# Kernel tuning notes

Hardware: AMD Instinct MI355X
Metric: run time of the kernel (lower is better)

The kernel has to match this reference:

```python
import jax, jax.numpy as jnp
import numpy as np

L, B, D = 50, 1024, 512      # memory slots, batch, d_model
H, DK = 4, 512               # heads, per-head dim (d_k = d_model in this module)
HOP = 3


def setup_inputs() -> dict:
    key = jax.random.key(0)
    ks = jax.random.split(key, 16)
    s = lambda i, shape: jax.random.normal(ks[i], shape, jnp.float32) * 0.02
    return dict(
        momery=jax.random.normal(ks[0], (L, B, D), jnp.float32),
        hid=jax.random.normal(ks[1], (B, D), jnp.float32),
        text_polarity=jax.random.normal(ks[2], (B,), jnp.float32),
        attribute_polarity=jax.random.normal(ks[3], (B,), jnp.float32),
        w=jnp.array(0.5, jnp.float32),
        p_w1=s(4, (D, D)), p_b1=jnp.zeros((D,), jnp.float32),
        p_w2=s(5, (D, D)), p_b2=jnp.zeros((D,), jnp.float32),
        wq=s(6, (D, H * DK)), bq=jnp.zeros((H * DK,), jnp.float32),
        wk=s(7, (D, H * DK)), bk=jnp.zeros((H * DK,), jnp.float32),
        wv=s(8, (D, H * DK)), bv=jnp.zeros((H * DK,), jnp.float32),
        wo=s(9, (H * DK, D)), bo=jnp.zeros((D,), jnp.float32),
    )


def reference(momery, hid, text_polarity, attribute_polarity, w,
              p_w1, p_b1, p_w2, p_b2, wq, bq, wk, bk, wv, bv, wo, bo):
    # k, v depend only on hid (attinkv = hid every hop/slot) -> hoist out of hop loop
    k = (hid @ wk + bk).reshape(B, H, DK)   # [B,H,DK]
    v = (hid @ wv + bv).reshape(B, H, DK)   # [B,H,DK]
    inv_sqrt_dk = jnp.float32(1.0 / np.sqrt(DK))
    for _ in range(HOP):
        # projection MLP over all slots at once (replaces per-slot loop)
        mid = jax.nn.relu(momery @ p_w1 + p_b1) @ p_w2 + p_b2          # [L,B,D]
        q = (mid @ wq + bq).reshape(L, B, H, DK)                        # [L,B,H,DK]
        # single key per query (nk=1): scores [L,B,H,1], softmax -> ones
        scores = (jnp.einsum('lbhd,bhd->lbh', q, k) * inv_sqrt_dk)[..., None]
        att = jax.nn.softmax(scores, axis=-1)                           # [L,B,H,1]
        out = att * v                                                   # [L,B,H,DK]
        temp = out.reshape(L, B, H * DK) @ wo + bo                      # [L,B,D]
        momery = momery + w * temp
    return momery
```

## Files before the change

### kernel.cpp

```cpp
#include <hip/hip_runtime.h>
#include <hip/hip_bf16.h>

typedef short short8 __attribute__((ext_vector_type(8)));
typedef float f4 __attribute__((ext_vector_type(4)));

__device__ __forceinline__ short f2bfs(float f) {
    __hip_bfloat16 h = __float2bfloat16(f);
    return __builtin_bit_cast(short, h);
}

__device__ __forceinline__ unsigned packbf2(float a, float b, float s) {
    unsigned lo = (unsigned short)f2bfs(s * a);
    unsigned hi = (unsigned short)f2bfs(s * b);
    return (hi << 16) | lo;
}

#define MFMA(a, b, c) __builtin_amdgcn_mfma_f32_16x16x32_bf16(a, b, c, 0, 0, 0)

__global__ __launch_bounds__(256) void gemmW(const float* __restrict__ wv,
                                             const float* __restrict__ wo,
                                             const float* __restrict__ bv,
                                             const float* __restrict__ bo,
                                             const float* __restrict__ w,
                                             short* __restrict__ WsT,
                                             float* __restrict__ b2p) {
    constexpr int K = 2048, N = 512, NT = 16;
    const int tid = threadIdx.x;
    const int bx  = blockIdx.x;

    if (bx >= 256) {
        const int g = (bx - 256) * 256 + tid;
        const int o = g & 511;
        const int r = g >> 9;
        float s = (r == 0) ? bo[o] : 0.f;
        const int j0 = r * 64;
#pragma unroll 8
        for (int j = j0; j < j0 + 64; ++j) s += bv[j] * wo[(size_t)j * N + o];
        b2p[r * 512 + o] = s;
        return;
    }

    __shared__ float red[4][32][33];

    const int row0 = (bx >> 4) * 32;
    const int col0 = (bx & 15) * 32;
    const int lane = tid & 63, wave = tid >> 6;
    const int ln = lane & 15, q = lane >> 4;
    const int k0 = wave * 512;

    const float* pa0 = wv + (size_t)(row0 + ln) * K + k0 + q * 8;
    const float* pa1 = pa0 + (size_t)16 * K;
    const float* pb  = wo + (size_t)(k0 + q * 8) * N;

    float4 a00 = *(const float4*)pa0, a01 = *(const float4*)(pa0 + 4);
    float4 a10 = *(const float4*)pa1, a11 = *(const float4*)(pa1 + 4);
    float b0r[8], b1r[8];
#pragma unroll
    for (int j = 0; j < 8; ++j) {
        b0r[j] = pb[(size_t)j * N + col0 + ln];
        b1r[j] = pb[(size_t)j * N + col0 + 16 + ln];
    }

    f4 acc00 = {0,0,0,0}, acc01 = {0,0,0,0}, acc10 = {0,0,0,0}, acc11 = {0,0,0,0};

    for (int t = 0; t < NT; ++t) {
        short8 af0, af1, bf0, bf1;
        af0[0]=f2bfs(a00.x); af0[1]=f2bfs(a00.y); af0[2]=f2bfs(a00.z); af0[3]=f2bfs(a00.w);
        af0[4]=f2bfs(a01.x); af0[5]=f2bfs(a01.y); af0[6]=f2bfs(a01.z); af0[7]=f2bfs(a01.w);
        af1[0]=f2bfs(a10.x); af1[1]=f2bfs(a10.y); af1[2]=f2bfs(a10.z); af1[3]=f2bfs(a10.w);
        af1[4]=f2bfs(a11.x); af1[5]=f2bfs(a11.y); af1[6]=f2bfs(a11.z); af1[7]=f2bfs(a11.w);
#pragma unroll
        for (int j = 0; j < 8; ++j) { bf0[j] = f2bfs(b0r[j]); bf1[j] = f2bfs(b1r[j]); }

        if (t + 1 < NT) {
            pa0 += 32; pa1 += 32; pb += (size_t)32 * N;
            a00 = *(const float4*)pa0; a01 = *(const float4*)(pa0 + 4);
            a10 = *(const float4*)pa1; a11 = *(const float4*)(pa1 + 4);
#pragma unroll
            for (int j = 0; j < 8; ++j) {
                b0r[j] = pb[(size_t)j * N + col0 + ln];
                b1r[j] = pb[(size_t)j * N + col0 + 16 + ln];
            }
        }
        acc00 = MFMA(af0, bf0, acc00); acc01 = MFMA(af0, bf1, acc01);
        acc10 = MFMA(af1, bf0, acc10); acc11 = MFMA(af1, bf1, acc11);
    }

#pragma unroll
    for (int r = 0; r < 4; ++r) {
        red[wave][q * 4 + r][ln]           = acc00[r];
        red[wave][q * 4 + r][ln + 16]      = acc01[r];
        red[wave][16 + q * 4 + r][ln]      = acc10[r];
        red[wave][16 + q * 4 + r][ln + 16] = acc11[r];
    }
    __syncthreads();

    const float wsc = 3.0f * w[0];
    const int n  = tid >> 3;
    const int d0 = (tid & 7) * 4;
    float s0 = red[0][d0][n]     + red[1][d0][n]     + red[2][d0][n]     + red[3][d0][n];
    float s1 = red[0][d0 + 1][n] + red[1][d0 + 1][n] + red[2][d0 + 1][n] + red[3][d0 + 1][n];
    float s2 = red[0][d0 + 2][n] + red[1][d0 + 2][n] + red[2][d0 + 2][n] + red[3][d0 + 2][n];
    float s3 = red[0][d0 + 3][n] + red[1][d0 + 3][n] + red[2][d0 + 3][n] + red[3][d0 + 3][n];
    short* p = WsT + (size_t)(col0 + n) * 512 + row0 + d0;
    *(unsigned*)p       = packbf2(s0, s1, wsc);
    *(unsigned*)(p + 2) = packbf2(s2, s3, wsc);
}

__global__ __launch_bounds__(256) void gemmT(const float* __restrict__ hid,
                                             const short* __restrict__ WsT,
                                             const float* __restrict__ b2p,
                                             const float* __restrict__ w,
                                             float* __restrict__ t) {
    constexpr int K = 512, N = 512, NT = 16;
    __shared__ float bred[4][64];

    const int tid  = threadIdx.x;
    const int col0 = blockIdx.x * 64;
    const int row0 = blockIdx.y * 32;
    const int lane = tid & 63, wave = tid >> 6;
    const int ln = lane & 15, q = lane >> 4;
    const int col = col0 + wave * 16 + ln;

    const int cl = tid & 63, rr = tid >> 6;
    const float* bpp = b2p + (size_t)(rr * 8) * 512 + col0 + cl;
    float bp = 0.f;
#pragma unroll
    for (int k = 0; k < 8; ++k) bp += bpp[(size_t)k * 512];

    const float* pa0 = hid + (size_t)(row0 + ln) * K + q * 8;
    const float* pa1 = pa0 + (size_t)16 * K;
    const short* pb  = WsT + (size_t)col * K + q * 8;

    float4 a00 = *(const float4*)pa0, a01 = *(const float4*)(pa0 + 4);
    float4 a10 = *(const float4*)pa1, a11 = *(const float4*)(pa1 + 4);
    short8 bf = *(const short8*)pb;

    f4 acc0 = {0,0,0,0}, acc1 = {0,0,0,0};

    for (int tt = 0; tt < NT; ++tt) {
        short8 af0, af1;
        af0[0]=f2bfs(a00.x); af0[1]=f2bfs(a00.y); af0[2]=f2bfs(a00.z); af0[3]=f2bfs(a00.w);
        af0[4]=f2bfs(a01.x); af0[5]=f2bfs(a01.y); af0[6]=f2bfs(a01.z); af0[7]=f2bfs(a01.w);
        af1[0]=f2bfs(a10.x); af1[1]=f2bfs(a10.y); af1[2]=f2bfs(a10.z); af1[3]=f2bfs(a10.w);
        af1[4]=f2bfs(a11.x); af1[5]=f2bfs(a11.y); af1[6]=f2bfs(a11.z); af1[7]=f2bfs(a11.w);
        short8 b = bf;
        if (tt + 1 < NT) {
            pa0 += 32; pa1 += 32; pb += 32;
            a00 = *(const float4*)pa0; a01 = *(const float4*)(pa0 + 4);
            a10 = *(const float4*)pa1; a11 = *(const float4*)(pa1 + 4);
            bf = *(const short8*)pb;
        }
        acc0 = MFMA(af0, b, acc0);
        acc1 = MFMA(af1, b, acc1);
    }

    bred[rr][cl] = bp;
    __syncthreads();
    const int lc = wave * 16 + ln;
    const float wsc  = 3.0f * w[0];
    const float bias = wsc * (bred[0][lc] + bred[1][lc] + bred[2][lc] + bred[3][lc]);

#pragma unroll
    for (int r = 0; r < 4; ++r) {
        t[(size_t)(row0 + q * 4 + r) * N + col]      = acc0[r] + bias;
        t[(size_t)(row0 + 16 + q * 4 + r) * N + col] = acc1[r] + bias;
    }
}

__global__ __launch_bounds__(256) void bcast(const float* __restrict__ mem,
                                             const float* __restrict__ t,
                                             float* __restrict__ out) {
    const size_t idx = (size_t)blockIdx.x * 256 + threadIdx.x;
    const int bd4 = (int)(idx & (131072 - 1));
    const f4 tv = ((const f4*)t)[bd4];
    const f4 m  = ((const f4*)mem)[idx];
    ((f4*)out)[idx] = m + tv;
}

extern "C" void kernel_launch(void* const* d_in, const int* in_sizes, int n_in,
                              void* d_out, int out_size, void* d_ws, size_t ws_size,
                              hipStream_t stream) {
    const float* momery = (const float*)d_in[0];
    const float* hid    = (const float*)d_in[1];
    const float* w      = (const float*)d_in[4];
    const float* wv     = (const float*)d_in[13];
    const float* bv     = (const float*)d_in[14];
    const float* wo     = (const float*)d_in[15];
    const float* bo     = (const float*)d_in[16];
    float* out = (float*)d_out;

    short* WsT = (short*)d_ws;
    float* b2p = (float*)(WsT + 262144);
    float* t   = b2p + 32 * 512;

    gemmW<<<320, 256, 0, stream>>>(wv, wo, bv, bo, w, WsT, b2p);
    gemmT<<<dim3(8, 32), 256, 0, stream>>>(hid, WsT, b2p, w, t);
    bcast<<<25600, 256, 0, stream>>>(momery, t, out);
}
```

Measured before the change: 241.4 us.

## Fuse weight-product and hid GEMMs into one cooperative kernel with grid sync

The separate gemmW and gemmT launches are merged into one cooperative kernel of 320 blocks. A grid-wide sync sits between the Wv·Wo product and the hid×WsT GEMM, which removes one kernel launch boundary. The broadcast-add kernel now uses nontemporal loads and stores for the large memory streams to avoid polluting the cache. Cooperative launch requires all 320 blocks to be co-resident, and the grid barrier adds its own sync cost.

```diff
diff --git a/kernel.cpp b/kernel.cpp
--- a/kernel.cpp
+++ b/kernel.cpp
@@ -1,5 +1,8 @@
 #include <hip/hip_runtime.h>
 #include <hip/hip_bf16.h>
+#include <hip/hip_cooperative_groups.h>
+
+namespace cg = cooperative_groups;
 
 typedef short short8 __attribute__((ext_vector_type(8)));
 typedef float f4 __attribute__((ext_vector_type(4)));
@@ -17,16 +20,23 @@
 
 #define MFMA(a, b, c) __builtin_amdgcn_mfma_f32_16x16x32_bf16(a, b, c, 0, 0, 0)
 
-__global__ __launch_bounds__(256) void gemmW(const float* __restrict__ wv,
-                                             const float* __restrict__ wo,
-                                             const float* __restrict__ bv,
-                                             const float* __restrict__ bo,
-                                             const float* __restrict__ w,
-                                             short* __restrict__ WsT,
-                                             float* __restrict__ b2p) {
+__global__ __launch_bounds__(256) void gemmWT(const float* __restrict__ wv,
+                                              const float* __restrict__ wo,
+                                              const float* __restrict__ bv,
+                                              const float* __restrict__ bo,
+                                              const float* __restrict__ w,
+                                              const float* __restrict__ hid,
+                                              short* __restrict__ WsT,
+                                              float* __restrict__ b2p,
+                                              float* __restrict__ t) {
     constexpr int K = 2048, N = 512, NT = 16;
+    __shared__ float red[4][32][33];
+    __shared__ float bred[4][64];
+
     const int tid = threadIdx.x;
     const int bx  = blockIdx.x;
+    const int lane = tid & 63, wave = tid >> 6;
+    const int ln = lane & 15, q = lane >> 4;
 
     if (bx >= 256) {
         const int g = (bx - 256) * 256 + tid;
@@ -37,89 +47,78 @@
 #pragma unroll 8
         for (int j = j0; j < j0 + 64; ++j) s += bv[j] * wo[(size_t)j * N + o];
         b2p[r * 512 + o] = s;
-        return;
+    } else {
+        const int row0 = (bx >> 4) * 32;
+        const int col0 = (bx & 15) * 32;
+        const int k0 = wave * 512;
+
+        const float* pa0 = wv + (size_t)(row0 + ln) * K + k0 + q * 8;
+        const float* pa1 = pa0 + (size_t)16 * K;
+        const float* pb  = wo + (size_t)(k0 + q * 8) * N;
+
+        float4 a00 = *(const float4*)pa0, a01 = *(const float4*)(pa0 + 4);
+        float4 a10 = *(const float4*)pa1, a11 = *(const float4*)(pa1 + 4);
+        float b0r[8], b1r[8];
+#pragma unroll
+        for (int j = 0; j < 8; ++j) {
+            b0r[j] = pb[(size_t)j * N + col0 + ln];
+            b1r[j] = pb[(size_t)j * N + col0 + 16 + ln];
+        }
+
+        f4 acc00 = {0,0,0,0}, acc01 = {0,0,0,0}, acc10 = {0,0,0,0}, acc11 = {0,0,0,0};
+
+        for (int tt = 0; tt < NT; ++tt) {
+            short8 af0, af1, bf0, bf1;
+            af0[0]=f2bfs(a00.x); af0[1]=f2bfs(a00.y); af0[2]=f2bfs(a00.z); af0[3]=f2bfs(a00.w);
+            af0[4]=f2bfs(a01.x); af0[5]=f2bfs(a01.y); af0[6]=f2bfs(a01.z); af0[7]=f2bfs(a01.w);
+            af1[0]=f2bfs(a10.x); af1[1]=f2bfs(a10.y); af1[2]=f2bfs(a10.z); af1[3]=f2bfs(a10.w);
+            af1[4]=f2bfs(a11.x); af1[5]=f2bfs(a11.y); af1[6]=f2bfs(a11.z); af1[7]=f2bfs(a11.w);
+#pragma unroll
+            for (int j = 0; j < 8; ++j) { bf0[j] = f2bfs(b0r[j]); bf1[j] = f2bfs(b1r[j]); }
+
+            if (tt + 1 < NT) {
+                pa0 += 32; pa1 += 32; pb += (size_t)32 * N;
+                a00 = *(const float4*)pa0; a01 = *(const float4*)(pa0 + 4);
+                a10 = *(const float4*)pa1; a11 = *(const float4*)(pa1 + 4);
+#pragma unroll
+                for (int j = 0; j < 8; ++j) {
+                    b0r[j] = pb[(size_t)j * N + col0 + ln];
+                    b1r[j] = pb[(size_t)j * N + col0 + 16 + ln];
+                }
+            }
+            acc00 = MFMA(af0, bf0, acc00); acc01 = MFMA(af0, bf1, acc01);
+            acc10 = MFMA(af1, bf0, acc10); acc11 = MFMA(af1, bf1, acc11);
+        }
+
+#pragma unroll
+        for (int r = 0; r < 4; ++r) {
+            red[wave][q * 4 + r][ln]           = acc00[r];
+            red[wave][q * 4 + r][ln + 16]      = acc01[r];
+            red[wave][16 + q * 4 + r][ln]      = acc10[r];
+            red[wave][16 + q * 4 + r][ln + 16] = acc11[r];
+        }
+        __syncthreads();
+
+        const float wsc = 3.0f * w[0];
+        const int n  = tid >> 3;
+        const int d0 = (tid & 7) * 4;
+        float s0 = red[0][d0][n]     + red[1][d0][n]     + red[2][d0][n]     + red[3][d0][n];
+        float s1 = red[0][d0 + 1][n] + red[1][d0 + 1][n] + red[2][d0 + 1][n] + red[3][d0 + 1][n];
+        float s2 = red[0][d0 + 2][n] + red[1][d0 + 2][n] + red[2][d0 + 2][n] + red[3][d0 + 2][n];
+        float s3 = red[0][d0 + 3][n] + red[1][d0 + 3][n] + red[2][d0 + 3][n] + red[3][d0 + 3][n];
+        short* p = WsT + (size_t)(col0 + n) * 512 + row0 + d0;
+        *(unsigned*)p       = packbf2(s0, s1, wsc);
+        *(unsigned*)(p + 2) = packbf2(s2, s3, wsc);
     }
 
-    __shared__ float red[4][32][33];
-
-    const int row0 = (bx >> 4) * 32;
-    const int col0 = (bx & 15) * 32;
-    const int lane = tid & 63, wave = tid >> 6;
-    const int ln = lane & 15, q = lane >> 4;
-    const int k0 = wave * 512;
-
-    const float* pa0 = wv + (size_t)(row0 + ln) * K + k0 + q * 8;
-    const float* pa1 = pa0 + (size_t)16 * K;
-    const float* pb  = wo + (size_t)(k0 + q * 8) * N;
-
-    float4 a00 = *(const float4*)pa0, a01 = *(const float4*)(pa0 + 4);
-    float4 a10 = *(const float4*)pa1, a11 = *(const float4*)(pa1 + 4);
-    float b0r[8], b1r[8];
-#pragma unroll
-    for (int j = 0; j < 8; ++j) {
-        b0r[j] = pb[(size_t)j * N + col0 + ln];
-        b1r[j] = pb[(size_t)j * N + col0 + 16 + ln];
-    }
-
-    f4 acc00 = {0,0,0,0}, acc01 = {0,0,0,0}, acc10 = {0,0,0,0}, acc11 = {0,0,0,0};
-
-    for (int t = 0; t < NT; ++t) {
-        short8 af0, af1, bf0, bf1;
-        af0[0]=f2bfs(a00.x); af0[1]=f2bfs(a00.y); af0[2]=f2bfs(a00.z); af0[3]=f2bfs(a00.w);
-        af0[4]=f2bfs(a01.x); af0[5]=f2bfs(a01.y); af0[6]=f2bfs(a01.z); af0[7]=f2bfs(a01.w);
-        af1[0]=f2bfs(a10.x); af1[1]=f2bfs(a10.y); af1[2]=f2bfs(a10.z); af1[3]=f2bfs(a10.w);
-        af1[4]=f2bfs(a11.x); af1[5]=f2bfs(a11.y); af1[6]=f2bfs(a11.z); af1[7]=f2bfs(a11.w);
-#pragma unroll
-        for (int j = 0; j < 8; ++j) { bf0[j] = f2bfs(b0r[j]); bf1[j] = f2bfs(b1r[j]); }
-
-        if (t + 1 < NT) {
-            pa0 += 32; pa1 += 32; pb += (size_t)32 * N;
-            a00 = *(const float4*)pa0; a01 = *(const float4*)(pa0 + 4);
-            a10 = *(const float4*)pa1; a11 = *(const float4*)(pa1 + 4);
-#pragma unroll
-            for (int j = 0; j < 8; ++j) {
-                b0r[j] = pb[(size_t)j * N + col0 + ln];
-                b1r[j] = pb[(size_t)j * N + col0 + 16 + ln];
-            }
-        }
-        acc00 = MFMA(af0, bf0, acc00); acc01 = MFMA(af0, bf1, acc01);
-        acc10 = MFMA(af1, bf0, acc10); acc11 = MFMA(af1, bf1, acc11);
-    }
-
-#pragma unroll
-    for (int r = 0; r < 4; ++r) {
-        red[wave][q * 4 + r][ln]           = acc00[r];
-        red[wave][q * 4 + r][ln + 16]      = acc01[r];
-        red[wave][16 + q * 4 + r][ln]      = acc10[r];
-        red[wave][16 + q * 4 + r][ln + 16] = acc11[r];
-    }
-    __syncthreads();
-
-    const float wsc = 3.0f * w[0];
-    const int n  = tid >> 3;
-    const int d0 = (tid & 7) * 4;
-    float s0 = red[0][d0][n]     + red[1][d0][n]     + red[2][d0][n]     + red[3][d0][n];
-    float s1 = red[0][d0 + 1][n] + red[1][d0 + 1][n] + red[2][d0 + 1][n] + red[3][d0 + 1][n];
-    float s2 = red[0][d0 + 2][n] + red[1][d0 + 2][n] + red[2][d0 + 2][n] + red[3][d0 + 2][n];
-    float s3 = red[0][d0 + 3][n] + red[1][d0 + 3][n] + red[2][d0 + 3][n] + red[3][d0 + 3][n];
-    short* p = WsT + (size_t)(col0 + n) * 512 + row0 + d0;
-    *(unsigned*)p       = packbf2(s0, s1, wsc);
-    *(unsigned*)(p + 2) = packbf2(s2, s3, wsc);
-}
-
-__global__ __launch_bounds__(256) void gemmT(const float* __restrict__ hid,
-                                             const short* __restrict__ WsT,
-                                             const float* __restrict__ b2p,
-                                             const float* __restrict__ w,
-                                             float* __restrict__ t) {
-    constexpr int K = 512, N = 512, NT = 16;
-    __shared__ float bred[4][64];
-
-    const int tid  = threadIdx.x;
-    const int col0 = blockIdx.x * 64;
-    const int row0 = blockIdx.y * 32;
-    const int lane = tid & 63, wave = tid >> 6;
-    const int ln = lane & 15, q = lane >> 4;
+    __threadfence();
+    cg::this_grid().sync();
+
+    if (bx >= 256) return;
+
+    constexpr int K2 = 512;
+    const int col0 = (bx & 7) * 64;
+    const int row0 = (bx >> 3) * 32;
     const int col = col0 + wave * 16 + ln;
 
     const int cl = tid & 63, rr = tid >> 6;
@@ -128,9 +127,9 @@
 #pragma unroll
     for (int k = 0; k < 8; ++k) bp += bpp[(size_t)k * 512];
 
-    const float* pa0 = hid + (size_t)(row0 + ln) * K + q * 8;
-    const float* pa1 = pa0 + (size_t)16 * K;
-    const short* pb  = WsT + (size_t)col * K + q * 8;
+    const float* pa0 = hid + (size_t)(row0 + ln) * K2 + q * 8;
+    const float* pa1 = pa0 + (size_t)16 * K2;
+    const short* pb  = WsT + (size_t)col * K2 + q * 8;
 
     float4 a00 = *(const float4*)pa0, a01 = *(const float4*)(pa0 + 4);
     float4 a10 = *(const float4*)pa1, a11 = *(const float4*)(pa1 + 4);
@@ -155,6 +154,7 @@
         acc1 = MFMA(af1, b, acc1);
     }
 
+    __syncthreads();
     bred[rr][cl] = bp;
     __syncthreads();
     const int lc = wave * 16 + ln;
@@ -174,8 +174,8 @@
     const size_t idx = (size_t)blockIdx.x * 256 + threadIdx.x;
     const int bd4 = (int)(idx & (131072 - 1));
     const f4 tv = ((const f4*)t)[bd4];
-    const f4 m  = ((const f4*)mem)[idx];
-    ((f4*)out)[idx] = m + tv;
+    const f4 m  = __builtin_nontemporal_load((const f4*)mem + idx);
+    __builtin_nontemporal_store(m + tv, (f4*)out + idx);
 }
 
 extern "C" void kernel_launch(void* const* d_in, const int* in_sizes, int n_in,
@@ -194,7 +194,10 @@
     float* b2p = (float*)(WsT + 262144);
     float* t   = b2p + 32 * 512;
 
-    gemmW<<<320, 256, 0, stream>>>(wv, wo, bv, bo, w, WsT, b2p);
-    gemmT<<<dim3(8, 32), 256, 0, stream>>>(hid, WsT, b2p, w, t);
+    void* args[] = {(void*)&wv, (void*)&wo, (void*)&bv, (void*)&bo, (void*)&w,
+                    (void*)&hid, (void*)&WsT, (void*)&b2p, (void*)&t};
+    hipLaunchCooperativeKernel((const void*)gemmWT, dim3(320), dim3(256),
+                               args, 0, stream);
+
     bcast<<<25600, 256, 0, stream>>>(momery, t, out);
 }
```

Measured after the change: 340.2 us. 40.9% more time.
